# Optimization experiments

Measured on AMD Instinct MI355X. Metric: run time of the kernel, lower is better.

The kernel has to match this reference:

```python
import jax, jax.numpy as jnp
import numpy as np

B, N, DIM = 2, 2048, 1024
H, DH = 16, 64
DIM_INNER = H * DH
EPS = float(jnp.finfo(jnp.float32).eps)  # torch nn.RMSNorm default eps = finfo.eps
THETA = 10000.0


def setup_inputs() -> dict:
    key = jax.random.key(0)
    ks = jax.random.split(key, 6)
    s = 0.02
    tokens = jax.random.normal(ks[0], (B, N, DIM), dtype=jnp.float32)
    w_norm = jnp.ones((DIM,), jnp.float32)                      # prenorm RMSNorm weight
    w_q = jax.random.normal(ks[1], (DIM, DIM_INNER), jnp.float32) * s
    w_k = jax.random.normal(ks[2], (DIM, 3 * DIM_INNER), jnp.float32) * s
    w_v = jax.random.normal(ks[3], (DIM, 3 * DIM_INNER), jnp.float32) * s
    w_key_norms = jnp.ones((3, DH), jnp.float32)                # 3 key RMSNorms
    w_nested_knorm = jnp.ones((DH,), jnp.float32)
    w_out = jax.random.normal(ks[4], (DIM_INNER, DIM), jnp.float32) * s
    return {"tokens": tokens, "w_norm": w_norm, "w_q": w_q, "w_k": w_k,
            "w_v": w_v, "w_key_norms": w_key_norms,
            "w_nested_knorm": w_nested_knorm, "w_out": w_out}


def rmsnorm(x, w):
    var = jnp.mean(jnp.square(x), axis=-1, keepdims=True)
    return x * jax.lax.rsqrt(var + EPS) * w


def rope(x):
    # interleaved (GPT-J style) rotary, as in rotary_embedding_torch defaults
    n, d = x.shape[-2], x.shape[-1]
    inv_freq = 1.0 / (THETA ** (jnp.arange(0, d, 2, dtype=jnp.float32) / d))
    freqs = jnp.arange(n, dtype=jnp.float32)[:, None] * inv_freq   # (n, d/2)
    cos = jnp.repeat(jnp.cos(freqs), 2, axis=-1)                   # (n, d)
    sin = jnp.repeat(jnp.sin(freqs), 2, axis=-1)
    x1, x2 = x[..., ::2], x[..., 1::2]
    x_rot = jnp.stack((-x2, x1), axis=-1).reshape(x.shape)         # rotate_half
    return x * cos + x_rot * sin


def attend(q, k, v):
    # rotate_queries_with_cached_keys with equal lengths -> plain rotary on both
    q = rope(q)
    k = rope(k)
    d = q.shape[-1]
    scores = jnp.einsum('bhqd,bhkd->bhqk', q, k) / jnp.sqrt(jnp.float32(d))
    n = scores.shape[-1]
    causal = jnp.tril(jnp.ones((n, n), dtype=bool))
    scores = jnp.where(causal, scores, -jnp.inf)
    attn = jax.nn.softmax(scores, axis=-1)
    return jnp.einsum('bhqk,bhkd->bhqd', attn, v)


def reference(tokens, w_norm, w_q, w_k, w_v, w_key_norms, w_nested_knorm, w_out):
    b, n = tokens.shape[:2]
    x = rmsnorm(tokens, w_norm)                                    # prenorm
    q = (x @ w_q).reshape(b, n, H, DH).transpose(0, 2, 1, 3)       # (b,h,n,d)
    # chunk(3, dim=-1) then split heads -> (3,b,h,n,d)
    ks = (x @ w_k).reshape(b, n, 3, H, DH).transpose(2, 0, 3, 1, 4)
    vs = (x @ w_v).reshape(b, n, 3, H, DH).transpose(2, 0, 3, 1, 4)
    ks = rmsnorm(ks, w_key_norms[:, None, None, None, :])          # per-branch key norm
    # three parallel causal attentions sharing the same queries
    nq, nk, nv = jax.vmap(attend, in_axes=(None, 0, 0))(q, ks, vs)
    nk = rmsnorm(nk, w_nested_knorm)
    out = attend(nq, nk, nv)                                       # nested attention
    out = out.transpose(0, 2, 1, 3).reshape(b, n, DIM_INNER)       # merge heads
    return out @ w_out
```

## Files before the change

### kernel.cpp

```cpp
#include <hip/hip_runtime.h>
#include <hip/hip_bf16.h>
#include <stdint.h>

typedef unsigned short u16;
typedef __attribute__((ext_vector_type(8))) short short8;
typedef __attribute__((ext_vector_type(4))) float float4v;
typedef __attribute__((ext_vector_type(4))) unsigned int uint4v;

#define B_    2
#define N_    2048
#define DIM_  1024
#define H_    16
#define DH_   64
#define DI_   1024
#define EPS_  1.1920928955078125e-07f
#define LOG2_THETA 13.287712379549449f
#define SCL_  0.18033688011112042f

__device__ __forceinline__ float bf2f(u16 u) {
    union { unsigned int i; float f; } v; v.i = ((unsigned int)u) << 16; return v.f;
}
__device__ __forceinline__ u16 f2bf(float f) {
    union { float f; unsigned int i; } v; v.f = f;
    unsigned int r = v.i + 0x7fff + ((v.i >> 16) & 1);
    return (u16)(r >> 16);
}
__device__ __forceinline__ unsigned int pack2bf(float a, float b) {
    union { float f; unsigned int i; } ua, ub; ua.f = a; ub.f = b;
    return ((ua.i + 0x8000u) >> 16) | ((ub.i + 0x8000u) & 0xffff0000u);
}
__device__ __forceinline__ int perm32(int n) {
    return (n & ~31) + (((n >> 2) & 3) * 8) + (((n >> 4) & 1) * 4) + (n & 3);
}

__global__ __launch_bounds__(256) void k_rmsnorm_x(
    const float* __restrict__ tok, const float* __restrict__ w, u16* __restrict__ xn) {
    int row = blockIdx.x;
    int t = threadIdx.x;
    const float* tr = tok + (size_t)row * DIM_;
    float vals[4];
    float ss = 0.f;
#pragma unroll
    for (int i = 0; i < 4; ++i) {
        float v = tr[t + i * 256];
        vals[i] = v; ss += v * v;
    }
#pragma unroll
    for (int o = 32; o; o >>= 1) ss += __shfl_xor(ss, o, 64);
    __shared__ float red[4];
    if ((t & 63) == 0) red[t >> 6] = ss;
    __syncthreads();
    ss = red[0] + red[1] + red[2] + red[3];
    float rs = rsqrtf(ss * (1.0f / DIM_) + EPS_);
    u16* orow = xn + (size_t)row * DIM_;
#pragma unroll
    for (int i = 0; i < 4; ++i) {
        int c = t + i * 256;
        orow[c] = f2bf(vals[i] * rs * w[c]);
    }
}

__global__ __launch_bounds__(256) void k_transpose(
    const float* __restrict__ src, u16* __restrict__ dst, int K, int N) {
    __shared__ float tile[32][33];
    int n0 = blockIdx.x * 32, k0 = blockIdx.y * 32;
    int tx = threadIdx.x, ty = threadIdx.y;
#pragma unroll
    for (int i = 0; i < 4; ++i)
        tile[ty + 8 * i][tx] = src[(size_t)(k0 + ty + 8 * i) * N + n0 + tx];
    __syncthreads();
#pragma unroll
    for (int i = 0; i < 4; ++i)
        dst[(size_t)(n0 + ty + 8 * i) * K + k0 + tx] = f2bf(tile[tx][ty + 8 * i]);
}

__global__ __launch_bounds__(256) void k_transpose_qkv(
    const float* __restrict__ w_q, const float* __restrict__ w_k,
    const float* __restrict__ w_v, u16* __restrict__ dst) {
    __shared__ float tile[32][33];
    int c0 = blockIdx.x * 32, k0 = blockIdx.y * 32;
    const float* src; int sN, sc0;
    if (c0 < 1024)      { src = w_q; sN = 1024; sc0 = c0; }
    else if (c0 < 4096) { src = w_k; sN = 3072; sc0 = c0 - 1024; }
    else                { src = w_v; sN = 3072; sc0 = c0 - 4096; }
    int tx = threadIdx.x, ty = threadIdx.y;
#pragma unroll
    for (int i = 0; i < 4; ++i)
        tile[ty + 8 * i][tx] = src[(size_t)(k0 + ty + 8 * i) * sN + sc0 + tx];
    __syncthreads();
#pragma unroll
    for (int i = 0; i < 4; ++i)
        dst[(size_t)(c0 + ty + 8 * i) * 1024 + k0 + tx] = f2bf(tile[tx][ty + 8 * i]);
}

__global__ __launch_bounds__(256) void k_transpose_v(
    const u16* __restrict__ QKVB, u16* __restrict__ Vt) {
    int y = blockIdx.y;
    int s = y >> 5;
    int b = (y >> 4) & 1;
    int h = y & 15;
    int n0 = blockIdx.x * 64;
    __shared__ u16 tile[64][72];
    int t = threadIdx.x;
#pragma unroll
    for (int i = 0; i < 2; ++i) {
        int idx = i * 256 + t;
        int row = idx >> 3, c = idx & 7;
        uint4v v = *(const uint4v*)(QKVB + ((size_t)(b * N_) + n0 + row) * 7168
                                        + 4096 + s * 1024 + h * 64 + c * 8);
        *(uint4v*)&tile[row][c * 8] = v;
    }
    __syncthreads();
    u16* out = Vt + (size_t)y * 64 * N_;
#pragma unroll
    for (int i = 0; i < 2; ++i) {
        int idx = i * 256 + t;
        int dh = idx >> 3, c = idx & 7;
#pragma unroll
        for (int j = 0; j < 8; ++j) {
            int n = c * 8 + j;
            out[(size_t)dh * N_ + n0 + perm32(n)] = tile[n][dh];
        }
    }
}

template <bool OUT_F32>
__global__ __launch_bounds__(256) void k_gemm_bt(
    const u16* __restrict__ A, const u16* __restrict__ Bt, void* __restrict__ Cv,
    int K, int Ncols) {
    __shared__ u16 As[128 * 32];
    __shared__ u16 Bs[128 * 32];
    int m0 = blockIdx.x * 128, n0 = blockIdx.y * 128;
    int t = threadIdx.x;
    int w = t >> 6, lane = t & 63, ln = lane & 15, quad = lane >> 4;
    int wm = w & 1, wn = w >> 1;
    float4v acc[4][4] = {};
    const u16* Ag = A + (size_t)m0 * K;
    const u16* Bg = Bt + (size_t)n0 * K;
    for (int k0 = 0; k0 < K; k0 += 32) {
        __syncthreads();
#pragma unroll
        for (int i = 0; i < 2; ++i) {
            int idx = i * 256 + t;
            int row = idx >> 2, kb = idx & 3;
            const u16* ga = Ag + (size_t)row * K + k0 + kb * 8;
            const u16* gb = Bg + (size_t)row * K + k0 + kb * 8;
            __builtin_amdgcn_global_load_lds(
                (const __attribute__((address_space(1))) void*)ga,
                (__attribute__((address_space(3))) void*)(As + idx * 8), 16, 0, 0);
            __builtin_amdgcn_global_load_lds(
                (const __attribute__((address_space(1))) void*)gb,
                (__attribute__((address_space(3))) void*)(Bs + idx * 8), 16, 0, 0);
        }
        asm volatile("s_waitcnt vmcnt(0)" ::: "memory");
        __syncthreads();
        short8 af[4], bfr[4];
#pragma unroll
        for (int mt = 0; mt < 4; ++mt)
            af[mt] = *(const short8*)(As + (wm * 64 + mt * 16 + ln) * 32 + quad * 8);
#pragma unroll
        for (int nt = 0; nt < 4; ++nt)
            bfr[nt] = *(const short8*)(Bs + (wn * 64 + nt * 16 + ln) * 32 + quad * 8);
#pragma unroll
        for (int mt = 0; mt < 4; ++mt)
#pragma unroll
            for (int nt = 0; nt < 4; ++nt)
                acc[mt][nt] = __builtin_amdgcn_mfma_f32_16x16x32_bf16(
                    af[mt], bfr[nt], acc[mt][nt], 0, 0, 0);
    }
#pragma unroll
    for (int mt = 0; mt < 4; ++mt)
#pragma unroll
        for (int nt = 0; nt < 4; ++nt)
#pragma unroll
            for (int r = 0; r < 4; ++r) {
                int row = m0 + wm * 64 + mt * 16 + quad * 4 + r;
                int col = n0 + wn * 64 + nt * 16 + ln;
                if (OUT_F32)
                    ((float*)Cv)[(size_t)row * Ncols + col] = acc[mt][nt][r];
                else
                    ((u16*)Cv)[(size_t)row * Ncols + col] = f2bf(acc[mt][nt][r]);
            }
}

__global__ __launch_bounds__(256) void k_rms_rope_k(
    u16* __restrict__ buf, const float* __restrict__ w,
    int row_stride, int col0, int nsets) {
    int vid = blockIdx.x * 4 + (threadIdx.x >> 6);
    int lane = threadIdx.x & 63;
    int h = vid % H_;
    int s = (vid / H_) % nsets;
    int row = vid / (H_ * nsets);
    int n = row & (N_ - 1);
    u16* p = buf + (size_t)row * row_stride + col0 + s * 1024 + h * 64;
    float x = bf2f(p[lane]);
    float ss = x * x;
#pragma unroll
    for (int o = 32; o; o >>= 1) ss += __shfl_xor(ss, o, 64);
    float rs = rsqrtf(ss * (1.0f / 64.0f) + EPS_);
    float xn = x * rs * w[s * 64 + lane];
    float partner = __shfl_xor(xn, 1, 64);
    float inv = exp2f(-(float)(lane & ~1) * (LOG2_THETA / 64.0f));
    float fr = (float)n * inv;
    float sv, cv;
    __sincosf(fr, &sv, &cv);
    float out = xn * cv + ((lane & 1) ? partner : -partner) * sv;
    p[lane] = f2bf(out);
}

__global__ __launch_bounds__(256, 3) void k_flash(
    const u16* __restrict__ Q, int q_stride,
    const u16* __restrict__ K, const u16* __restrict__ Vt,
    u16* __restrict__ O, u16* __restrict__ Ot,
    int kv_stride, int set_off, size_t o_set_stride) {
    int bh = blockIdx.x;
    int qt = gridDim.y - 1 - blockIdx.y;
    int s = blockIdx.z;
    int b = bh >> 4, h = bh & 15;
    int t = threadIdx.x;
    int w = t >> 6, lane = t & 63, ln = lane & 15, quad = lane >> 4;
    int lnx = ln & 7;
    int q0 = qt * 128;
    int qw = q0 + w * 32;

    const u16* Qb  = Q + ((size_t)b * N_) * q_stride + h * 64;
    const u16* Kb  = K + ((size_t)b * N_) * kv_stride + (size_t)s * set_off + h * 64;
    const u16* Vtb = Vt + (size_t)((s * B_ + b) * H_ + h) * (64 * (size_t)N_);

    __shared__ u16 Ks[2][64][64];
    __shared__ u16 Vs[2][64][64];

    short8 ones;
#pragma unroll
    for (int j = 0; j < 8; ++j) ((u16*)&ones)[j] = 0x3F80;

    short8 qf[2][2];
    float mrow[2];
    float4v accO[2][4] = {};
    float4v accL[2] = {};
#pragma unroll
    for (int g = 0; g < 2; ++g) {
        int qg = qw + g * 16;
        int tokn = qg + ln;
        short8 raw[2];
#pragma unroll
        for (int f = 0; f < 2; ++f)
            raw[f] = *(const short8*)(Qb + (size_t)tokn * q_stride + f * 32 + quad * 8);
        float qn = 0.f;
#pragma unroll
        for (int f = 0; f < 2; ++f)
#pragma unroll
            for (int j = 0; j < 8; ++j) {
                float v = bf2f(((const u16*)&raw[f])[j]);
                qn += v * v;
            }
        qn += __shfl_xor(qn, 16, 64);
        qn += __shfl_xor(qn, 32, 64);
        mrow[g] = sqrtf(qn) * (8.0f * SCL_) * 1.03f + 1e-6f;
#pragma unroll
        for (int f = 0; f < 2; ++f) {
            u16 out8[8];
            int dbase = f * 32 + quad * 8;
#pragma unroll
            for (int tp = 0; tp < 4; ++tp) {
                int d = dbase + 2 * tp;
                float inv = exp2f((float)d * (-LOG2_THETA / 64.0f));
                float fr = (float)tokn * inv;
                float sv, cv;
                __sincosf(fr, &sv, &cv);
                float x0 = bf2f(((const u16*)&raw[f])[2 * tp]);
                float x1 = bf2f(((const u16*)&raw[f])[2 * tp + 1]);
                out8[2 * tp]     = f2bf((x0 * cv - x1 * sv) * SCL_);
                out8[2 * tp + 1] = f2bf((x1 * cv + x0 * sv) * SCL_);
            }
            qf[g][f] = *(const short8*)out8;
        }
    }

    int ntb = 2 * qt + 2;

    auto stage = [&](int kt0, int buf) {
        int k0 = kt0 * 64;
#pragma unroll
        for (int i = 0; i < 2; ++i) {
            int idx = i * 256 + t;
            int row = idx >> 3, c = idx & 7;
            int csrc = ((c ^ (row & 7)) * 8);
            const u16* ga = Kb + (size_t)(k0 + row) * kv_stride + csrc;
            __builtin_amdgcn_global_load_lds(
                (const __attribute__((address_space(1))) void*)ga,
                (__attribute__((address_space(3))) void*)&Ks[buf][row][c * 8], 16, 0, 0);
            const u16* gv = Vtb + (size_t)row * N_ + k0 + csrc;
            __builtin_amdgcn_global_load_lds(
                (const __attribute__((address_space(1))) void*)gv,
                (__attribute__((address_space(3))) void*)&Vs[buf][row][c * 8], 16, 0, 0);
        }
    };
    stage(0, 0);

    for (int kt0 = 0; kt0 < ntb; ++kt0) {
        asm volatile("s_waitcnt vmcnt(0)" ::: "memory");
        __syncthreads();
        if (kt0 + 1 < ntb) stage(kt0 + 1, (kt0 + 1) & 1);
        int buf = kt0 & 1;
        int k0 = kt0 * 64;
        if (k0 > qw + 31) continue;

        short8 kf[4][2];
#pragma unroll
        for (int kt = 0; kt < 4; ++kt) {
            const u16* krow = &Ks[buf][kt * 16 + ln][0];
            kf[kt][0] = *(const short8*)(krow + ((quad ^ lnx) * 8));
            kf[kt][1] = *(const short8*)(krow + (((4 + quad) ^ lnx) * 8));
        }

        short8 pb[2][2];
#pragma unroll
        for (int g = 0; g < 2; ++g) {
            int qg = qw + g * 16;
            float4v st[4];
#pragma unroll
            for (int kt = 0; kt < 4; ++kt) {
                float4v sa = {-mrow[g], -mrow[g], -mrow[g], -mrow[g]};
                sa = __builtin_amdgcn_mfma_f32_16x16x32_bf16(kf[kt][0], qf[g][0], sa, 0, 0, 0);
                sa = __builtin_amdgcn_mfma_f32_16x16x32_bf16(kf[kt][1], qf[g][1], sa, 0, 0, 0);
                st[kt] = sa;
            }
            if (k0 + 63 <= qg) {
#pragma unroll
                for (int c = 0; c < 2; ++c) {
                    uint4v pk;
#pragma unroll
                    for (int kt2 = 0; kt2 < 2; ++kt2) {
                        float e0 = exp2f(st[c * 2 + kt2][0]);
                        float e1 = exp2f(st[c * 2 + kt2][1]);
                        float e2 = exp2f(st[c * 2 + kt2][2]);
                        float e3 = exp2f(st[c * 2 + kt2][3]);
                        pk[kt2 * 2 + 0] = pack2bf(e0, e1);
                        pk[kt2 * 2 + 1] = pack2bf(e2, e3);
                    }
                    pb[g][c] = *(short8*)&pk;
                }
            } else {
                int qr = qg + ln;
#pragma unroll
                for (int c = 0; c < 2; ++c) {
                    uint4v pk;
#pragma unroll
                    for (int kt2 = 0; kt2 < 2; ++kt2) {
                        int kt = c * 2 + kt2;
                        float e[4];
#pragma unroll
                        for (int r = 0; r < 4; ++r) {
                            int kg = k0 + kt * 16 + quad * 4 + r;
                            float arg = (kg <= qr) ? st[kt][r] : -1e30f;
                            e[r] = exp2f(arg);
                        }
                        pk[kt2 * 2 + 0] = pack2bf(e[0], e[1]);
                        pk[kt2 * 2 + 1] = pack2bf(e[2], e[3]);
                    }
                    pb[g][c] = *(short8*)&pk;
                }
            }
        }

#pragma unroll
        for (int dc = 0; dc < 4; ++dc) {
            const u16* vrow = &Vs[buf][dc * 16 + ln][0];
            short8 vf0 = *(const short8*)(vrow + ((quad ^ lnx) * 8));
            short8 vf1 = *(const short8*)(vrow + (((4 + quad) ^ lnx) * 8));
#pragma unroll
            for (int g = 0; g < 2; ++g) {
                accO[g][dc] = __builtin_amdgcn_mfma_f32_16x16x32_bf16(vf0, pb[g][0], accO[g][dc], 0, 0, 0);
                accO[g][dc] = __builtin_amdgcn_mfma_f32_16x16x32_bf16(vf1, pb[g][1], accO[g][dc], 0, 0, 0);
            }
        }
#pragma unroll
        for (int g = 0; g < 2; ++g) {
            accL[g] = __builtin_amdgcn_mfma_f32_16x16x32_bf16(ones, pb[g][0], accL[g], 0, 0, 0);
            accL[g] = __builtin_amdgcn_mfma_f32_16x16x32_bf16(ones, pb[g][1], accL[g], 0, 0, 0);
        }
    }

#pragma unroll
    for (int g = 0; g < 2; ++g) {
        float rinv = 1.0f / accL[g][0];
        int qg = qw + g * 16;
        int qr = qg + ln;
        if (s == 2) {
            u16* Otb = Ot + (size_t)(b * H_ + h) * (64 * (size_t)N_);
            int pos = perm32(qr & (N_ - 1)) + (qr & ~(N_ - 1));
#pragma unroll
            for (int dc = 0; dc < 4; ++dc)
#pragma unroll
                for (int r = 0; r < 4; ++r)
                    Otb[(size_t)(dc * 16 + quad * 4 + r) * N_ + pos] =
                        f2bf(accO[g][dc][r] * rinv);
        } else {
            u16* Ob = O + (size_t)s * o_set_stride + ((size_t)b * N_) * DI_ + h * 64;
#pragma unroll
            for (int dc = 0; dc < 4; ++dc) {
                uint2 pk;
                pk.x = pack2bf(accO[g][dc][0] * rinv, accO[g][dc][1] * rinv);
                pk.y = pack2bf(accO[g][dc][2] * rinv, accO[g][dc][3] * rinv);
                *(uint2*)(Ob + (size_t)qr * DI_ + dc * 16 + quad * 4) = pk;
            }
        }
    }
}

extern "C" void kernel_launch(void* const* d_in, const int* in_sizes, int n_in,
                              void* d_out, int out_size, void* d_ws, size_t ws_size,
                              hipStream_t stream) {
    const float* tok     = (const float*)d_in[0];
    const float* w_norm  = (const float*)d_in[1];
    const float* w_q     = (const float*)d_in[2];
    const float* w_k     = (const float*)d_in[3];
    const float* w_v     = (const float*)d_in[4];
    const float* w_keyn  = (const float*)d_in[5];
    const float* w_nestk = (const float*)d_in[6];
    const float* w_o     = (const float*)d_in[7];

    char* ws = (char*)d_ws;
    const size_t MB = 1024 * 1024;
    u16* QKVB  = (u16*)(ws + 0 * MB);
    u16* VtB   = (u16*)(ws + 56 * MB);
    u16* NQKV  = (u16*)(ws + 80 * MB);
    u16* WQKVT = (u16*)(ws + 80 * MB);
    u16* NVt   = (u16*)(ws + 96 * MB);
    u16* XN    = (u16*)(ws + 96 * MB);
    u16* OUT2  = (u16*)(ws + 104 * MB);
    u16* WOT   = (u16*)(ws + 80 * MB);

    const size_t SET = (size_t)B_ * N_ * DI_;

    k_transpose_qkv<<<dim3(224, 32), dim3(32, 8), 0, stream>>>(w_q, w_k, w_v, WQKVT);

    k_rmsnorm_x<<<B_ * N_, 256, 0, stream>>>(tok, w_norm, XN);

    k_gemm_bt<false><<<dim3(32, 56), 256, 0, stream>>>(XN, WQKVT, QKVB, 1024, 7168);

    k_transpose_v<<<dim3(N_ / 64, 3 * B_ * H_), 256, 0, stream>>>(QKVB, VtB);

    k_rms_rope_k<<<(B_ * N_ * 3 * H_) / 4, 256, 0, stream>>>(QKVB, w_keyn, 7168, 1024, 3);

    k_flash<<<dim3(B_ * H_, N_ / 128, 3), 256, 0, stream>>>(
        QKVB, 7168, QKVB + 1024, VtB, NQKV, NVt, 7168, 1024, SET);

    k_rms_rope_k<<<(B_ * N_ * H_) / 4, 256, 0, stream>>>(NQKV + SET, w_nestk, 1024, 0, 1);

    k_flash<<<dim3(B_ * H_, N_ / 128, 1), 256, 0, stream>>>(
        NQKV, 1024, NQKV + SET, NVt, OUT2, NVt , 1024, 0, 0);

    k_transpose<<<dim3(32, 32), dim3(32, 8), 0, stream>>>(w_o, WOT, 1024, 1024);
    k_gemm_bt<true><<<dim3(32, 8), 256, 0, stream>>>(OUT2, WOT, (float*)d_out, 1024, 1024);
}
```

Measured before the change: 443.1 us.

## Load K/V fragments directly from global memory in flash kernel, drop LDS staging

Removes the shared-memory double-buffered K/V staging and block-wide barriers from the flash-attention kernel. Each wave now loads its MFMA K and V fragments straight from global memory and loops only over the key tiles it needs. It also swaps the manual bf16 packing for the hardware v_cvt_pk_bf16_f32 instruction. The aim is to cut barrier stalls and per-wave causal imbalance. The cost is that the four waves no longer share K/V loads, so global and L2 traffic rises and load latency is no longer hidden by prefetch.

```diff
diff --git a/kernel.cpp b/kernel.cpp
--- a/kernel.cpp
+++ b/kernel.cpp
@@ -28,6 +28,11 @@
 __device__ __forceinline__ unsigned int pack2bf(float a, float b) {
     union { float f; unsigned int i; } ua, ub; ua.f = a; ub.f = b;
     return ((ua.i + 0x8000u) >> 16) | ((ub.i + 0x8000u) & 0xffff0000u);
+}
+__device__ __forceinline__ unsigned int cvtpk(float a, float b) {
+    unsigned int r;
+    asm("v_cvt_pk_bf16_f32 %0, %1, %2" : "=v"(r) : "v"(a), "v"(b));
+    return r;
 }
 __device__ __forceinline__ int perm32(int n) {
     return (n & ~31) + (((n >> 2) & 3) * 8) + (((n >> 4) & 1) * 4) + (n & 3);
@@ -219,16 +224,12 @@
     int b = bh >> 4, h = bh & 15;
     int t = threadIdx.x;
     int w = t >> 6, lane = t & 63, ln = lane & 15, quad = lane >> 4;
-    int lnx = ln & 7;
     int q0 = qt * 128;
     int qw = q0 + w * 32;
 
     const u16* Qb  = Q + ((size_t)b * N_) * q_stride + h * 64;
     const u16* Kb  = K + ((size_t)b * N_) * kv_stride + (size_t)s * set_off + h * 64;
     const u16* Vtb = Vt + (size_t)((s * B_ + b) * H_ + h) * (64 * (size_t)N_);
-
-    __shared__ u16 Ks[2][64][64];
-    __shared__ u16 Vs[2][64][64];
 
     short8 ones;
 #pragma unroll
@@ -277,41 +278,20 @@
         }
     }
 
-    int ntb = 2 * qt + 2;
-
-    auto stage = [&](int kt0, int buf) {
+    int ntw = (qw >> 6) + 1;
+
+    const u16* KbL = Kb + (size_t)ln * kv_stride + quad * 8;
+    const u16* VtL = Vtb + (size_t)ln * N_ + quad * 8;
+
+    for (int kt0 = 0; kt0 < ntw; ++kt0) {
         int k0 = kt0 * 64;
-#pragma unroll
-        for (int i = 0; i < 2; ++i) {
-            int idx = i * 256 + t;
-            int row = idx >> 3, c = idx & 7;
-            int csrc = ((c ^ (row & 7)) * 8);
-            const u16* ga = Kb + (size_t)(k0 + row) * kv_stride + csrc;
-            __builtin_amdgcn_global_load_lds(
-                (const __attribute__((address_space(1))) void*)ga,
-                (__attribute__((address_space(3))) void*)&Ks[buf][row][c * 8], 16, 0, 0);
-            const u16* gv = Vtb + (size_t)row * N_ + k0 + csrc;
-            __builtin_amdgcn_global_load_lds(
-                (const __attribute__((address_space(1))) void*)gv,
-                (__attribute__((address_space(3))) void*)&Vs[buf][row][c * 8], 16, 0, 0);
-        }
-    };
-    stage(0, 0);
-
-    for (int kt0 = 0; kt0 < ntb; ++kt0) {
-        asm volatile("s_waitcnt vmcnt(0)" ::: "memory");
-        __syncthreads();
-        if (kt0 + 1 < ntb) stage(kt0 + 1, (kt0 + 1) & 1);
-        int buf = kt0 & 1;
-        int k0 = kt0 * 64;
-        if (k0 > qw + 31) continue;
 
         short8 kf[4][2];
 #pragma unroll
         for (int kt = 0; kt < 4; ++kt) {
-            const u16* krow = &Ks[buf][kt * 16 + ln][0];
-            kf[kt][0] = *(const short8*)(krow + ((quad ^ lnx) * 8));
-            kf[kt][1] = *(const short8*)(krow + (((4 + quad) ^ lnx) * 8));
+            const u16* krow = KbL + (size_t)(k0 + kt * 16) * kv_stride;
+            kf[kt][0] = *(const short8*)(krow);
+            kf[kt][1] = *(const short8*)(krow + 32);
         }
 
         short8 pb[2][2];
@@ -332,12 +312,10 @@
                     uint4v pk;
 #pragma unroll
                     for (int kt2 = 0; kt2 < 2; ++kt2) {
-                        float e0 = exp2f(st[c * 2 + kt2][0]);
-                        float e1 = exp2f(st[c * 2 + kt2][1]);
-                        float e2 = exp2f(st[c * 2 + kt2][2]);
-                        float e3 = exp2f(st[c * 2 + kt2][3]);
-                        pk[kt2 * 2 + 0] = pack2bf(e0, e1);
-                        pk[kt2 * 2 + 1] = pack2bf(e2, e3);
+                        pk[kt2 * 2 + 0] = cvtpk(exp2f(st[c * 2 + kt2][0]),
+                                                exp2f(st[c * 2 + kt2][1]));
+                        pk[kt2 * 2 + 1] = cvtpk(exp2f(st[c * 2 + kt2][2]),
+                                                exp2f(st[c * 2 + kt2][3]));
                     }
                     pb[g][c] = *(short8*)&pk;
                 }
@@ -356,8 +334,8 @@
                             float arg = (kg <= qr) ? st[kt][r] : -1e30f;
                             e[r] = exp2f(arg);
                         }
-                        pk[kt2 * 2 + 0] = pack2bf(e[0], e[1]);
-                        pk[kt2 * 2 + 1] = pack2bf(e[2], e[3]);
+                        pk[kt2 * 2 + 0] = cvtpk(e[0], e[1]);
+                        pk[kt2 * 2 + 1] = cvtpk(e[2], e[3]);
                     }
                     pb[g][c] = *(short8*)&pk;
                 }
@@ -366,9 +344,9 @@
 
 #pragma unroll
         for (int dc = 0; dc < 4; ++dc) {
-            const u16* vrow = &Vs[buf][dc * 16 + ln][0];
-            short8 vf0 = *(const short8*)(vrow + ((quad ^ lnx) * 8));
-            short8 vf1 = *(const short8*)(vrow + (((4 + quad) ^ lnx) * 8));
+            const u16* vrow = VtL + (size_t)(dc * 16) * N_ + k0;
+            short8 vf0 = *(const short8*)(vrow);
+            short8 vf1 = *(const short8*)(vrow + 32);
 #pragma unroll
             for (int g = 0; g < 2; ++g) {
                 accO[g][dc] = __builtin_amdgcn_mfma_f32_16x16x32_bf16(vf0, pb[g][0], accO[g][dc], 0, 0, 0);
@@ -401,8 +379,8 @@
 #pragma unroll
             for (int dc = 0; dc < 4; ++dc) {
                 uint2 pk;
-                pk.x = pack2bf(accO[g][dc][0] * rinv, accO[g][dc][1] * rinv);
-                pk.y = pack2bf(accO[g][dc][2] * rinv, accO[g][dc][3] * rinv);
+                pk.x = cvtpk(accO[g][dc][0] * rinv, accO[g][dc][1] * rinv);
+                pk.y = cvtpk(accO[g][dc][2] * rinv, accO[g][dc][3] * rinv);
                 *(uint2*)(Ob + (size_t)qr * DI_ + dc * 16 + quad * 4) = pk;
             }
         }
```

Result: slower. 627.6 us (+41.6%).
